# Performance work log

Measured on AMD Instinct MI355X. Metric: run time of the kernel, lower is better.

Reference implementation:

```python
import jax, jax.numpy as jnp
import numpy as np

F = 16  # ConvLSTM2D filters

def hard_sigmoid(x):
    # Keras (TF2) hard_sigmoid: clip(0.2*x + 0.5, 0, 1) -- ConvLSTM2D default recurrent_activation
    return jnp.clip(0.2 * x + 0.5, 0.0, 1.0)

def convlstm_1x1(x, W, U, b, reverse):
    # x: [B,T,H,W,C]; W: [C,4F]; U: [F,4F]; b: [4F]
    # 1x1 ConvLSTM2D == per-pixel LSTM; gate order in Keras kernel: i, f, c, o
    B, T, H, Wd, C = x.shape
    xs = jnp.moveaxis(x, 1, 0)  # [T,B,H,W,C]
    h0 = jnp.zeros((B, H, Wd, F), x.dtype)
    c0 = jnp.zeros((B, H, Wd, F), x.dtype)
    def step(carry, xt):
        h, c = carry
        z = jnp.einsum('bhwc,cf->bhwf', xt, W) + jnp.einsum('bhwc,cf->bhwf', h, U) + b
        i, f, g, o = jnp.split(z, 4, axis=-1)
        i = hard_sigmoid(i); f = hard_sigmoid(f); o = hard_sigmoid(o)
        c_new = f * c + i * jnp.tanh(g)
        h_new = o * jnp.tanh(c_new)
        return (h_new, c_new), h_new
    # reverse=True: scan runs backward in time, ys aligned to input order,
    # which matches Keras Bidirectional(go_backwards + output re-reversal).
    _, hs = jax.lax.scan(step, (h0, c0), xs, reverse=reverse)
    return jnp.moveaxis(hs, 0, 1)  # [B,T,H,W,F]

def setup_inputs() -> dict:
    key = jax.random.key(0)
    ks = jax.random.split(key, 13)
    B, T, H, Wd, C = 16, 64, 32, 32, 32
    s = 0.1
    inp = {
        'inputs': jax.random.normal(ks[0], (B, T, H, Wd, C), jnp.float32),
        'Wf': jax.random.normal(ks[1], (C, 4 * F), jnp.float32) * s,
        'Uf': jax.random.normal(ks[2], (F, 4 * F), jnp.float32) * s,
        'bf': jnp.zeros((4 * F,), jnp.float32),
        'Wb': jax.random.normal(ks[3], (C, 4 * F), jnp.float32) * s,
        'Ub': jax.random.normal(ks[4], (F, 4 * F), jnp.float32) * s,
        'bb': jnp.zeros((4 * F,), jnp.float32),
        'w1': jax.random.normal(ks[5], (2 * F, 16), jnp.float32) * s,
        'b1': jnp.zeros((16,), jnp.float32),
        'w2': jax.random.normal(ks[6], (16, 16), jnp.float32) * s,
        'b2': jnp.zeros((16,), jnp.float32),
        'w3': jax.random.normal(ks[7], (16, 10), jnp.float32) * s,
        'b3': jnp.zeros((10,), jnp.float32),
    }
    return inp

def reference(inputs, Wf, Uf, bf, Wb, Ub, bb, w1, b1, w2, b2, w3, b3):
    h_fwd = convlstm_1x1(inputs, Wf, Uf, bf, reverse=False)
    h_bwd = convlstm_1x1(inputs, Wb, Ub, bb, reverse=True)
    x = jnp.concatenate([h_fwd, h_bwd], axis=-1)  # [B,T,H,W,2F]
    x = jnp.einsum('...c,cd->...d', x, w1) + b1
    x = jnp.einsum('...c,cd->...d', x, w2) + b2
    x = jnp.einsum('...c,cd->...d', x, w3) + b3
    return x  # [B,T,H,W,10]
```

## Files before the change

### kernel.cpp

```cpp
#include <hip/hip_runtime.h>
#include <hip/hip_bf16.h>
#include <cstdint>
#include <cstddef>

#define TT 64
#define CC 32
#define FF 16
#define HWSZ 1024
#define NPIX 16384

typedef __attribute__((ext_vector_type(8))) short  short8;
typedef __attribute__((ext_vector_type(4))) float  f32x4;

__device__ __forceinline__ float bf2f(unsigned int u16) {
  union { unsigned int u; float f; } c;
  c.u = u16 << 16;
  return c.f;
}
__device__ __forceinline__ unsigned int f2bf(float f) {
  union { float f; unsigned int u; } c;
  c.f = f;
  unsigned int u = c.u;
  return (u + 0x7fffu + ((u >> 16) & 1u)) >> 16;
}
__device__ __forceinline__ float clamp01(float x) {
  return fminf(fmaxf(x, 0.0f), 1.0f);
}
__device__ __forceinline__ float tanhf_fast(float x) {
  float e = __expf(2.0f * x);
  return 1.0f - 2.0f / (e + 1.0f);
}

__global__ __launch_bounds__(512) void fold_kernel(
    const float* __restrict__ w1, const float* __restrict__ b1,
    const float* __restrict__ w2, const float* __restrict__ b2,
    const float* __restrict__ w3, const float* __restrict__ b3,
    float* __restrict__ Wc, float* __restrict__ bc)
{
  __shared__ float w23[16 * 10];
  __shared__ float bb2[16];
  const int t = threadIdx.x;

  if (t < 160) {
    const int k = t / 10, j = t % 10;
    float s = 0.0f;
    #pragma unroll
    for (int m = 0; m < 16; ++m) s = fmaf(w2[k * 16 + m], w3[m * 10 + j], s);
    w23[t] = s;
  }
  if (t < 16) {
    float s = b2[t];
    #pragma unroll
    for (int m = 0; m < 16; ++m) s = fmaf(b1[m], w2[m * 16 + t], s);
    bb2[t] = s;
  }
  __syncthreads();
  if (t < 320) {
    const int k = t / 10, j = t % 10;
    float s = 0.0f;
    #pragma unroll
    for (int m = 0; m < 16; ++m) s = fmaf(w1[k * 16 + m], w23[m * 10 + j], s);
    Wc[t] = s;
  }
  if (t < 10) {
    float s = b3[t];
    #pragma unroll
    for (int m = 0; m < 16; ++m) s = fmaf(bb2[m], w3[m * 10 + t], s);
    bc[t] = s;
  }
}

__global__ __launch_bounds__(256) void lstm_kernel(
    const float* __restrict__ x,
    const float* __restrict__ Wf, const float* __restrict__ Uf, const float* __restrict__ bfp,
    const float* __restrict__ Wb, const float* __restrict__ Ub, const float* __restrict__ bbp,
    unsigned short* __restrict__ hf_out, unsigned short* __restrict__ hb_out)
{
  const int dir = blockIdx.y;
  const float* __restrict__ Wp = dir ? Wb : Wf;
  const float* __restrict__ Up = dir ? Ub : Uf;
  const float* __restrict__ bp = dir ? bbp : bfp;
  unsigned short* __restrict__ hout = dir ? hb_out : hf_out;

  const int tid  = threadIdx.x;
  const int lane = tid & 63;
  const int wid  = tid >> 6;
  const int quad = lane >> 4;
  const int l15  = lane & 15;

  __shared__ unsigned short hst[4 * 16 * 40];
  unsigned short* hwv = hst + wid * 16 * 40;
  for (int i = tid; i < 4 * 16 * 40; i += 256) hst[i] = 0;
  __syncthreads();

  const int px  = (blockIdx.x * 4 + wid) * 16 + l15;
  const int b   = px >> 10;
  const int hwi = px & 1023;

  short8 Bx[4], Bu[4];
  #pragma unroll
  for (int nt = 0; nt < 4; ++nt) {
    short8 vx, vu;
    #pragma unroll
    for (int j = 0; j < 8; ++j) {
      const int k   = quad * 8 + j;
      const int col = nt * 16 + l15;
      vx[j] = (short)f2bf(Wp[k * 64 + col]);
      vu[j] = (k < FF) ? (short)f2bf(Up[k * 64 + col]) : (short)0;
    }
    Bx[nt] = vx; Bu[nt] = vu;
  }
  const float bi = fmaf(bp[ 0 + l15], 0.2f, 0.5f);
  const float bf = fmaf(bp[16 + l15], 0.2f, 0.5f);
  const float bg = bp[32 + l15];
  const float bo = fmaf(bp[48 + l15], 0.2f, 0.5f);

  float cst[4] = {0.f, 0.f, 0.f, 0.f};
  const int rd_off = l15 * 40 + quad * 8;
  int t_prev = 0;

  for (int s = 0; s < TT; ++s) {
    const int t = dir ? (TT - 1 - s) : s;
    const size_t pos = (size_t)(b * TT + t) * HWSZ + hwi;

    const float* xp = x + pos * CC + quad * 8;
    const float4 x0 = *reinterpret_cast<const float4*>(xp);
    const float4 x1 = *reinterpret_cast<const float4*>(xp + 4);
    short8 ax;
    ax[0] = (short)f2bf(x0.x); ax[1] = (short)f2bf(x0.y);
    ax[2] = (short)f2bf(x0.z); ax[3] = (short)f2bf(x0.w);
    ax[4] = (short)f2bf(x1.x); ax[5] = (short)f2bf(x1.y);
    ax[6] = (short)f2bf(x1.z); ax[7] = (short)f2bf(x1.w);

    const short8 ah = *reinterpret_cast<const short8*>(hwv + rd_off);

    if (s > 0 && lane < 32) {
      const size_t pprev = (size_t)(b * TT + t_prev) * HWSZ + hwi;
      *reinterpret_cast<short8*>(hout + pprev * 16 + quad * 8) = ah;
    }

    f32x4 zi = {0.f, 0.f, 0.f, 0.f}, zf = zi, zg = zi, zo = zi;
    zi = __builtin_amdgcn_mfma_f32_16x16x32_bf16(ax, Bx[0], zi, 0, 0, 0);
    zf = __builtin_amdgcn_mfma_f32_16x16x32_bf16(ax, Bx[1], zf, 0, 0, 0);
    zg = __builtin_amdgcn_mfma_f32_16x16x32_bf16(ax, Bx[2], zg, 0, 0, 0);
    zo = __builtin_amdgcn_mfma_f32_16x16x32_bf16(ax, Bx[3], zo, 0, 0, 0);
    zi = __builtin_amdgcn_mfma_f32_16x16x32_bf16(ah, Bu[0], zi, 0, 0, 0);
    zf = __builtin_amdgcn_mfma_f32_16x16x32_bf16(ah, Bu[1], zf, 0, 0, 0);
    zg = __builtin_amdgcn_mfma_f32_16x16x32_bf16(ah, Bu[2], zg, 0, 0, 0);
    zo = __builtin_amdgcn_mfma_f32_16x16x32_bf16(ah, Bu[3], zo, 0, 0, 0);

    #pragma unroll
    for (int r = 0; r < 4; ++r) {
      const float ig = clamp01(fmaf(zi[r], 0.2f, bi));
      const float fg = clamp01(fmaf(zf[r], 0.2f, bf));
      const float og = clamp01(fmaf(zo[r], 0.2f, bo));
      const float gg = tanhf_fast(zg[r] + bg);
      cst[r] = fmaf(fg, cst[r], ig * gg);
      const float hv = og * tanhf_fast(cst[r]);
      hwv[(quad * 4 + r) * 40 + l15] = (unsigned short)f2bf(hv);
    }
    t_prev = t;
  }

  const short8 ahf = *reinterpret_cast<const short8*>(hwv + rd_off);
  if (lane < 32) {
    const size_t pprev = (size_t)(b * TT + t_prev) * HWSZ + hwi;
    *reinterpret_cast<short8*>(hout + pprev * 16 + quad * 8) = ahf;
  }
}

__global__ __launch_bounds__(256) void dense_kernel(
    const unsigned short* __restrict__ hf, const unsigned short* __restrict__ hb,
    const float* __restrict__ Wc, const float* __restrict__ bc,
    float* __restrict__ out)
{
  __shared__ float w[320];
  __shared__ float bb[10];
  for (int i = threadIdx.x; i < 320; i += 256) w[i] = Wc[i];
  if (threadIdx.x < 10) bb[threadIdx.x] = bc[threadIdx.x];
  __syncthreads();

  const size_t pos = (size_t)blockIdx.x * 256 + threadIdx.x;

  const uint4* hf4 = reinterpret_cast<const uint4*>(hf) + pos * 2;
  const uint4* hb4 = reinterpret_cast<const uint4*>(hb) + pos * 2;
  uint4 q0 = hf4[0], q1 = hf4[1], q2 = hb4[0], q3 = hb4[1];
  unsigned int uw[16] = {q0.x, q0.y, q0.z, q0.w, q1.x, q1.y, q1.z, q1.w,
                         q2.x, q2.y, q2.z, q2.w, q3.x, q3.y, q3.z, q3.w};
  float hin[32];
  #pragma unroll
  for (int i = 0; i < 16; ++i) {
    hin[2 * i]     = bf2f(uw[i] & 0xffffu);
    hin[2 * i + 1] = bf2f(uw[i] >> 16);
  }

  float acc[10];
  #pragma unroll
  for (int j = 0; j < 10; ++j) acc[j] = bb[j];
  #pragma unroll
  for (int k = 0; k < 32; ++k) {
    const float v = hin[k];
    #pragma unroll
    for (int j = 0; j < 10; ++j) acc[j] = fmaf(v, w[k * 10 + j], acc[j]);
  }

  float2* o2 = reinterpret_cast<float2*>(out + pos * 10);
  o2[0] = make_float2(acc[0], acc[1]);
  o2[1] = make_float2(acc[2], acc[3]);
  o2[2] = make_float2(acc[4], acc[5]);
  o2[3] = make_float2(acc[6], acc[7]);
  o2[4] = make_float2(acc[8], acc[9]);
}

extern "C" void kernel_launch(void* const* d_in, const int* in_sizes, int n_in,
                              void* d_out, int out_size, void* d_ws, size_t ws_size,
                              hipStream_t stream) {
  const float* x   = (const float*)d_in[0];
  const float* Wf  = (const float*)d_in[1];
  const float* Uf  = (const float*)d_in[2];
  const float* bfp = (const float*)d_in[3];
  const float* Wb  = (const float*)d_in[4];
  const float* Ub  = (const float*)d_in[5];
  const float* bbp = (const float*)d_in[6];
  const float* w1  = (const float*)d_in[7];
  const float* b1  = (const float*)d_in[8];
  const float* w2  = (const float*)d_in[9];
  const float* b2  = (const float*)d_in[10];
  const float* w3  = (const float*)d_in[11];
  const float* b3  = (const float*)d_in[12];

  unsigned short* hfbuf = (unsigned short*)d_ws;
  unsigned short* hbbuf = hfbuf + (size_t)NPIX * TT * FF;
  float* Wc = (float*)(hbbuf + (size_t)NPIX * TT * FF);
  float* bc = Wc + 320;

  fold_kernel<<<1, 512, 0, stream>>>(w1, b1, w2, b2, w3, b3, Wc, bc);

  lstm_kernel<<<dim3(256, 2), 256, 0, stream>>>(x, Wf, Uf, bfp, Wb, Ub, bbp, hfbuf, hbbuf);

  const int npos = NPIX * TT;
  dense_kernel<<<npos / 256, 256, 0, stream>>>(hfbuf, hbbuf, Wc, bc, (float*)d_out);
}
```

Baseline: 299.2 us.

## Prefetch x, use exp2/rcp tanh, packed bf16 converts, MFMA dense head

The LSTM kernel now loads the next timestep's x one iteration ahead and walks it with incremental 32-bit byte offsets. Its tanh uses exp2 with a prescaled argument and a hardware reciprocal, and bf16 packing uses the paired conversion intrinsic. The dense head is rewritten to use bf16 MFMA, splitting the folded weights into hi and lo bf16 parts so the weights keep near-fp32 accuracy. Each wave handles 8 tiles of 16 positions, and 2048 blocks are launched instead of one thread per position. The costs are approximate tanh precision, 32-bit offsets that could overflow on larger inputs, and output stores of 10 floats per row that coalesce less well.

After: 282.9 us. -5.4%, faster.

```diff
diff --git a/kernel.cpp b/kernel.cpp
--- a/kernel.cpp
+++ b/kernel.cpp
@@ -23,12 +23,21 @@
   unsigned int u = c.u;
   return (u + 0x7fffu + ((u >> 16) & 1u)) >> 16;
 }
+__device__ __forceinline__ unsigned int pkbf(float a, float b) {
+  float2 f2; f2.x = a; f2.y = b;
+  __hip_bfloat162 h = __float22bfloat162_rn(f2);
+  union { __hip_bfloat162 h; unsigned int u; } c; c.h = h;
+  return c.u;
+}
 __device__ __forceinline__ float clamp01(float x) {
   return fminf(fmaxf(x, 0.0f), 1.0f);
 }
-__device__ __forceinline__ float tanhf_fast(float x) {
-  float e = __expf(2.0f * x);
-  return 1.0f - 2.0f / (e + 1.0f);
+
+#define L2E2 2.8853900817779268f
+__device__ __forceinline__ float tanh_e2(float e2arg) {
+  const float e = __builtin_exp2f(e2arg);
+  const float t = __builtin_amdgcn_rcpf(e + 1.0f);
+  return fmaf(-2.0f, t, 1.0f);
 }
 
 __global__ __launch_bounds__(512) void fold_kernel(
@@ -110,62 +119,80 @@
     }
     Bx[nt] = vx; Bu[nt] = vu;
   }
-  const float bi = fmaf(bp[ 0 + l15], 0.2f, 0.5f);
-  const float bf = fmaf(bp[16 + l15], 0.2f, 0.5f);
-  const float bg = bp[32 + l15];
-  const float bo = fmaf(bp[48 + l15], 0.2f, 0.5f);
+  const float bi  = fmaf(bp[ 0 + l15], 0.2f, 0.5f);
+  const float bf  = fmaf(bp[16 + l15], 0.2f, 0.5f);
+  const float bgl = bp[32 + l15] * L2E2;
+  const float bo  = fmaf(bp[48 + l15], 0.2f, 0.5f);
 
   float cst[4] = {0.f, 0.f, 0.f, 0.f};
   const int rd_off = l15 * 40 + quad * 8;
-  int t_prev = 0;
+
+  const int t0 = dir ? (TT - 1) : 0;
+  const unsigned int pos0 = (unsigned int)((b * TT + t0) * HWSZ + hwi);
+  unsigned int xoff = pos0 * (CC * 4) + quad * 32;
+  const int xstep = dir ? -(HWSZ * CC * 4) : (HWSZ * CC * 4);
+  unsigned int hob = pos0 * 32 + quad * 16;
+  const int hstep = dir ? -(HWSZ * 32) : (HWSZ * 32);
+  unsigned int hob_prev = hob;
+
+  const char* xb = (const char*)x;
+  char* hbb = (char*)hout;
+
+  float4 x0 = *reinterpret_cast<const float4*>(xb + xoff);
+  float4 x1 = *reinterpret_cast<const float4*>(xb + xoff + 16);
 
   for (int s = 0; s < TT; ++s) {
-    const int t = dir ? (TT - 1 - s) : s;
-    const size_t pos = (size_t)(b * TT + t) * HWSZ + hwi;
-
-    const float* xp = x + pos * CC + quad * 8;
-    const float4 x0 = *reinterpret_cast<const float4*>(xp);
-    const float4 x1 = *reinterpret_cast<const float4*>(xp + 4);
-    short8 ax;
-    ax[0] = (short)f2bf(x0.x); ax[1] = (short)f2bf(x0.y);
-    ax[2] = (short)f2bf(x0.z); ax[3] = (short)f2bf(x0.w);
-    ax[4] = (short)f2bf(x1.x); ax[5] = (short)f2bf(x1.y);
-    ax[6] = (short)f2bf(x1.z); ax[7] = (short)f2bf(x1.w);
+    union { short8 s8; unsigned int u[4]; } ax;
+    ax.u[0] = pkbf(x0.x, x0.y); ax.u[1] = pkbf(x0.z, x0.w);
+    ax.u[2] = pkbf(x1.x, x1.y); ax.u[3] = pkbf(x1.z, x1.w);
+
+    if (s + 1 < TT) {
+      xoff += xstep;
+      x0 = *reinterpret_cast<const float4*>(xb + xoff);
+      x1 = *reinterpret_cast<const float4*>(xb + xoff + 16);
+    }
 
     const short8 ah = *reinterpret_cast<const short8*>(hwv + rd_off);
 
     if (s > 0 && lane < 32) {
-      const size_t pprev = (size_t)(b * TT + t_prev) * HWSZ + hwi;
-      *reinterpret_cast<short8*>(hout + pprev * 16 + quad * 8) = ah;
+      *reinterpret_cast<short8*>(hbb + hob_prev) = ah;
     }
 
     f32x4 zi = {0.f, 0.f, 0.f, 0.f}, zf = zi, zg = zi, zo = zi;
-    zi = __builtin_amdgcn_mfma_f32_16x16x32_bf16(ax, Bx[0], zi, 0, 0, 0);
-    zf = __builtin_amdgcn_mfma_f32_16x16x32_bf16(ax, Bx[1], zf, 0, 0, 0);
-    zg = __builtin_amdgcn_mfma_f32_16x16x32_bf16(ax, Bx[2], zg, 0, 0, 0);
-    zo = __builtin_amdgcn_mfma_f32_16x16x32_bf16(ax, Bx[3], zo, 0, 0, 0);
+    zi = __builtin_amdgcn_mfma_f32_16x16x32_bf16(ax.s8, Bx[0], zi, 0, 0, 0);
+    zf = __builtin_amdgcn_mfma_f32_16x16x32_bf16(ax.s8, Bx[1], zf, 0, 0, 0);
+    zg = __builtin_amdgcn_mfma_f32_16x16x32_bf16(ax.s8, Bx[2], zg, 0, 0, 0);
+    zo = __builtin_amdgcn_mfma_f32_16x16x32_bf16(ax.s8, Bx[3], zo, 0, 0, 0);
     zi = __builtin_amdgcn_mfma_f32_16x16x32_bf16(ah, Bu[0], zi, 0, 0, 0);
     zf = __builtin_amdgcn_mfma_f32_16x16x32_bf16(ah, Bu[1], zf, 0, 0, 0);
     zg = __builtin_amdgcn_mfma_f32_16x16x32_bf16(ah, Bu[2], zg, 0, 0, 0);
     zo = __builtin_amdgcn_mfma_f32_16x16x32_bf16(ah, Bu[3], zo, 0, 0, 0);
 
+    float hv[4];
     #pragma unroll
     for (int r = 0; r < 4; ++r) {
       const float ig = clamp01(fmaf(zi[r], 0.2f, bi));
       const float fg = clamp01(fmaf(zf[r], 0.2f, bf));
       const float og = clamp01(fmaf(zo[r], 0.2f, bo));
-      const float gg = tanhf_fast(zg[r] + bg);
+      const float gg = tanh_e2(fmaf(zg[r], L2E2, bgl));
       cst[r] = fmaf(fg, cst[r], ig * gg);
-      const float hv = og * tanhf_fast(cst[r]);
-      hwv[(quad * 4 + r) * 40 + l15] = (unsigned short)f2bf(hv);
-    }
-    t_prev = t;
+      hv[r]  = og * tanh_e2(cst[r] * L2E2);
+    }
+    const unsigned int p01 = pkbf(hv[0], hv[1]);
+    const unsigned int p23 = pkbf(hv[2], hv[3]);
+    const int wr = quad * 4 * 40 + l15;
+    hwv[wr          ] = (unsigned short)(p01 & 0xffffu);
+    hwv[wr + 40     ] = (unsigned short)(p01 >> 16);
+    hwv[wr + 80     ] = (unsigned short)(p23 & 0xffffu);
+    hwv[wr + 120    ] = (unsigned short)(p23 >> 16);
+
+    hob_prev = hob;
+    hob += hstep;
   }
 
   const short8 ahf = *reinterpret_cast<const short8*>(hwv + rd_off);
   if (lane < 32) {
-    const size_t pprev = (size_t)(b * TT + t_prev) * HWSZ + hwi;
-    *reinterpret_cast<short8*>(hout + pprev * 16 + quad * 8) = ahf;
+    *reinterpret_cast<short8*>(hbb + hob_prev) = ahf;
   }
 }
 
@@ -174,42 +201,46 @@
     const float* __restrict__ Wc, const float* __restrict__ bc,
     float* __restrict__ out)
 {
-  __shared__ float w[320];
-  __shared__ float bb[10];
-  for (int i = threadIdx.x; i < 320; i += 256) w[i] = Wc[i];
-  if (threadIdx.x < 10) bb[threadIdx.x] = bc[threadIdx.x];
-  __syncthreads();
-
-  const size_t pos = (size_t)blockIdx.x * 256 + threadIdx.x;
-
-  const uint4* hf4 = reinterpret_cast<const uint4*>(hf) + pos * 2;
-  const uint4* hb4 = reinterpret_cast<const uint4*>(hb) + pos * 2;
-  uint4 q0 = hf4[0], q1 = hf4[1], q2 = hb4[0], q3 = hb4[1];
-  unsigned int uw[16] = {q0.x, q0.y, q0.z, q0.w, q1.x, q1.y, q1.z, q1.w,
-                         q2.x, q2.y, q2.z, q2.w, q3.x, q3.y, q3.z, q3.w};
-  float hin[32];
+  const int tid  = threadIdx.x;
+  const int lane = tid & 63;
+  const int quad = lane >> 4;
+  const int l15  = lane & 15;
+
+  short8 Bhi, Blo;
   #pragma unroll
-  for (int i = 0; i < 16; ++i) {
-    hin[2 * i]     = bf2f(uw[i] & 0xffffu);
-    hin[2 * i + 1] = bf2f(uw[i] >> 16);
-  }
-
-  float acc[10];
+  for (int j = 0; j < 8; ++j) {
+    const int k = quad * 8 + j;
+    const float v  = (l15 < 10) ? Wc[k * 10 + l15] : 0.0f;
+    const unsigned int hi = f2bf(v);
+    const float lo = v - bf2f(hi);
+    Bhi[j] = (short)hi;
+    Blo[j] = (short)f2bf(lo);
+  }
+  const float bcv = (l15 < 10) ? bc[l15] : 0.0f;
+
+  const unsigned short* __restrict__ src = (quad & 2) ? hb : hf;
+  const unsigned int lsub = (quad & 1) * 8;
+
+  const unsigned int gw = (blockIdx.x * 256 + tid) >> 6;
+
   #pragma unroll
-  for (int j = 0; j < 10; ++j) acc[j] = bb[j];
-  #pragma unroll
-  for (int k = 0; k < 32; ++k) {
-    const float v = hin[k];
-    #pragma unroll
-    for (int j = 0; j < 10; ++j) acc[j] = fmaf(v, w[k * 10 + j], acc[j]);
-  }
-
-  float2* o2 = reinterpret_cast<float2*>(out + pos * 10);
-  o2[0] = make_float2(acc[0], acc[1]);
-  o2[1] = make_float2(acc[2], acc[3]);
-  o2[2] = make_float2(acc[4], acc[5]);
-  o2[3] = make_float2(acc[6], acc[7]);
-  o2[4] = make_float2(acc[8], acc[9]);
+  for (int i = 0; i < 8; ++i) {
+    const unsigned int tile  = gw * 8 + i;
+    const unsigned int pos16 = tile * 16 + l15;
+    const short8 A = *reinterpret_cast<const short8*>(src + pos16 * 16 + lsub);
+
+    f32x4 acc = {bcv, bcv, bcv, bcv};
+    acc = __builtin_amdgcn_mfma_f32_16x16x32_bf16(A, Bhi, acc, 0, 0, 0);
+    acc = __builtin_amdgcn_mfma_f32_16x16x32_bf16(A, Blo, acc, 0, 0, 0);
+
+    if (l15 < 10) {
+      const unsigned int rowbase = tile * 16 + quad * 4;
+      #pragma unroll
+      for (int r = 0; r < 4; ++r) {
+        out[(size_t)(rowbase + r) * 10 + l15] = acc[r];
+      }
+    }
+  }
 }
 
 extern "C" void kernel_launch(void* const* d_in, const int* in_sizes, int n_in,
@@ -238,6 +269,5 @@
 
   lstm_kernel<<<dim3(256, 2), 256, 0, stream>>>(x, Wf, Uf, bfp, Wb, Ub, bbp, hfbuf, hbbuf);
 
-  const int npos = NPIX * TT;
-  dense_kernel<<<npos / 256, 256, 0, stream>>>(hfbuf, hbbuf, Wc, bc, (float*)d_out);
-}
+  dense_kernel<<<2048, 256, 0, stream>>>(hfbuf, hbbuf, Wc, bc, (float*)d_out);
+}
```
